# Kernel optimization log

Hardware: AMD Instinct MI355X
Metric: run time of the kernel (lower is better)

The kernel has to match this reference:

```python
import jax, jax.numpy as jnp
import numpy as np

EPS = 1e-5

def bn_eval(x, p):
    # p: [4, C] = gamma, beta, running_mean, running_var; channel-last broadcast
    g, b, m, v = p[0], p[1], p[2], p[3]
    return (x - m) * (g / jnp.sqrt(v + EPS)) + b

def _bn_params(k, c):
    k1, k2, k3, k4 = jax.random.split(k, 4)
    gamma = jax.random.uniform(k1, (c,)) + 0.5
    beta = jax.random.normal(k2, (c,)) * 0.1
    mean = jax.random.normal(k3, (c,)) * 0.1
    var = jax.random.uniform(k4, (c,)) + 0.5
    return jnp.stack([gamma, beta, mean, var])

def _lin(k, fan_in, fan_out):
    bound = 1.0 / np.sqrt(fan_in)
    kw, kb = jax.random.split(k)
    w = jax.random.uniform(kw, (fan_in, fan_out), minval=-bound, maxval=bound)
    b = jax.random.uniform(kb, (fan_out,), minval=-bound, maxval=bound)
    return w, b

def setup_inputs() -> dict:
    key = jax.random.key(0)
    B, N, S, C, G = 2, 4096, 16, 256, 8
    ks = jax.random.split(key, 20)
    feats = jax.random.normal(ks[0], (B, N, C), dtype=jnp.float32)
    coords = jax.random.normal(ks[1], (B, N, 3), dtype=jnp.float32)
    index = jax.random.randint(ks[2], (B, N, S), 0, N, dtype=jnp.int32)
    wq, bq = _lin(ks[3], C, C); bnq = _bn_params(ks[4], C)
    wk, bk = _lin(ks[5], C, C); bnk = _bn_params(ks[6], C)
    wv, bv = _lin(ks[7], C, C)
    pm_w1, pm_b1 = _lin(ks[8], 3, C); pm_bn = _bn_params(ks[9], C)
    pm_w2, pm_b2 = _lin(ks[10], C, C)
    pb_w1, pb_b1 = _lin(ks[11], 3, C); pb_bn = _bn_params(ks[12], C)
    pb_w2, pb_b2 = _lin(ks[13], C, C)
    we_w1, we_b1 = _lin(ks[14], C, G); we_bn = _bn_params(ks[15], G)
    we_w2, we_b2 = _lin(ks[16], G, G)
    return dict(feats=feats, coords=coords, index=index,
                wq=wq, bq=bq, bnq=bnq, wk=wk, bk=bk, bnk=bnk, wv=wv, bv=bv,
                pm_w1=pm_w1, pm_b1=pm_b1, pm_bn=pm_bn, pm_w2=pm_w2, pm_b2=pm_b2,
                pb_w1=pb_w1, pb_b1=pb_b1, pb_bn=pb_bn, pb_w2=pb_w2, pb_b2=pb_b2,
                we_w1=we_w1, we_b1=we_b1, we_bn=we_bn, we_w2=we_w2, we_b2=we_b2)

def reference(feats, coords, index,
              wq, bq, bnq, wk, bk, bnk, wv, bv,
              pm_w1, pm_b1, pm_bn, pm_w2, pm_b2,
              pb_w1, pb_b1, pb_bn, pb_w2, pb_b2,
              we_w1, we_b1, we_bn, we_w2, we_b2):
    B, N, C = feats.shape
    S = index.shape[2]
    G = we_w1.shape[1]
    q = jax.nn.relu(bn_eval(feats @ wq + bq, bnq))                       # [B,N,C]
    k = jax.nn.relu(bn_eval(feats @ wk + bk, bnk))                       # [B,N,C]
    v = feats @ wv + bv                                                   # [B,N,C]
    idx = index.reshape(B, N * S)
    key_g = jnp.take_along_axis(k, idx[:, :, None], axis=1).reshape(B, N, S, C)
    val_g = jnp.take_along_axis(v, idx[:, :, None], axis=1).reshape(B, N, S, C)
    crd_g = jnp.take_along_axis(coords, idx[:, :, None], axis=1).reshape(B, N, S, 3)
    relation_qk = key_g - q[:, :, None, :]                                # [B,N,S,C]
    pos = coords[:, :, None, :] - crd_g                                   # [B,N,S,3]
    pem = jax.nn.relu(bn_eval(pos @ pm_w1 + pm_b1, pm_bn)) @ pm_w2 + pm_b2
    relation_qk = relation_qk * pem
    peb = jax.nn.relu(bn_eval(pos @ pb_w1 + pb_b1, pb_bn)) @ pb_w2 + pb_b2
    relation_qk = relation_qk + peb
    val_g = val_g + peb
    w = jax.nn.relu(bn_eval(relation_qk @ we_w1 + we_b1, we_bn)) @ we_w2 + we_b2  # [B,N,S,G]
    w = jax.nn.softmax(w, axis=2)                                         # softmax over neighbors
    val_g = val_g.reshape(B, N, S, G, C // G)
    out = jnp.einsum('bnsgi,bnsg->bngi', val_g, w).reshape(B, N, C)
    return out
```

## Files before the change

kernel.cpp:

```cpp
#include <hip/hip_runtime.h>
#include <hip/hip_bf16.h>


typedef __attribute__((ext_vector_type(8))) short bf16x8_t;
typedef __attribute__((ext_vector_type(4))) float f32x4_t;

#define BN_EPS 1e-5f
#define WSYNC() asm volatile("s_waitcnt lgkmcnt(0)" ::: "memory")

__device__ __forceinline__ float blo(unsigned int v) {
    union { unsigned int u; float f; } x; x.u = v << 16; return x.f;
}
__device__ __forceinline__ float bhi(unsigned int v) {
    union { unsigned int u; float f; } x; x.u = v & 0xffff0000u; return x.f;
}
__device__ __forceinline__ unsigned int fbits(float f) {
    union { float f; unsigned int u; } x; x.f = f; return x.u;
}
__device__ __forceinline__ unsigned short f2b(float f) {
    unsigned int u = fbits(f);
    return (unsigned short)((u + 0x7fffu + ((u >> 16) & 1u)) >> 16);
}
__device__ __forceinline__ float b2f(unsigned short h) {
    union { unsigned int u; float f; } x; x.u = ((unsigned int)h) << 16; return x.f;
}
__device__ __forceinline__ unsigned int f2bpk(float a, float b) {
    union { __hip_bfloat162 h; unsigned int u; } x;
    x.h = __float22bfloat162_rn(make_float2(a, b));
    return x.u;
}
__device__ __forceinline__ unsigned int relpair(unsigned int kb, unsigned int qb,
                                                unsigned int pm_, unsigned int pb_) {
    float r0 = (blo(kb) - blo(qb)) * blo(pm_) + blo(pb_);
    float r1 = (bhi(kb) - bhi(qb)) * bhi(pm_) + bhi(pb_);
    return f2bpk(r0, r1);
}

__global__ __launch_bounds__(256) void k_prep(
    const float* __restrict__ wq, const float* __restrict__ wk,
    const float* __restrict__ wv, const float* __restrict__ pm2,
    const float* __restrict__ pb2,
    const float* __restrict__ pm_w1, const float* __restrict__ pm_b1,
    const float* __restrict__ pm_bn,
    const float* __restrict__ pb_w1, const float* __restrict__ pb_b1,
    const float* __restrict__ pb_bn,
    const float* __restrict__ we_w1,
    const float* __restrict__ bq, const float* __restrict__ bnq,
    const float* __restrict__ bk, const float* __restrict__ bnk,
    const float* __restrict__ bv,
    unsigned short* __restrict__ wsT, unsigned short* __restrict__ w1F,
    unsigned short* __restrict__ we1TF, float* __restrict__ SS)
{
    const int bid = blockIdx.x, t = threadIdx.x;
    if (bid < 160) {
        __shared__ unsigned short T[32][72];
        const int mat = bid >> 5;
        const int kk  = (bid >> 2) & 7;
        const int ntq = bid & 3;
        const float* s = (mat == 0) ? wq : (mat == 1) ? wk : (mat == 2) ? wv
                         : (mat == 3) ? pm2 : pb2;
        {
            int c = t & 63, r0 = t >> 6;
            for (int i = 0; i < 8; ++i) {
                int r = r0 + i * 4;
                T[r][c] = f2b(s[(kk * 32 + r) * 256 + ntq * 64 + c]);
            }
        }
        __syncthreads();
        {
            int seg = t >> 6, lane = t & 63;
            int col = seg * 16 + (lane & 15);
            int kr  = (lane >> 4) * 8;
            unsigned int v[8];
            #pragma unroll
            for (int j = 0; j < 8; ++j) v[j] = T[kr + j][col];
            uint4 o;
            o.x = v[0] | (v[1] << 16);
            o.y = v[2] | (v[3] << 16);
            o.z = v[4] | (v[5] << 16);
            o.w = v[6] | (v[7] << 16);
            *(uint4*)(wsT + mat * 65536 + (ntq * 4 + seg) * 4096 + kk * 512 + lane * 8) = o;
        }
    } else if (bid == 160) {
        int c = t;
        int nt = c >> 4, l15 = c & 15;
        float sm = pm_bn[c] / sqrtf(pm_bn[768 + c] + BN_EPS);
        float sb = pb_bn[c] / sqrtf(pb_bn[768 + c] + BN_EPS);
        float W[2][4];
        W[0][0] = pm_w1[c] * sm; W[0][1] = pm_w1[256 + c] * sm;
        W[0][2] = pm_w1[512 + c] * sm;
        W[0][3] = (pm_b1[c] - pm_bn[512 + c]) * sm + pm_bn[256 + c];
        W[1][0] = pb_w1[c] * sb; W[1][1] = pb_w1[256 + c] * sb;
        W[1][2] = pb_w1[512 + c] * sb;
        W[1][3] = (pb_b1[c] - pb_bn[512 + c]) * sb + pb_bn[256 + c];
        for (int pass = 0; pass < 2; ++pass) {
            unsigned short xh = f2b(W[pass][0]), xl = f2b(W[pass][0] - b2f(xh));
            unsigned short yh = f2b(W[pass][1]), yl = f2b(W[pass][1] - b2f(yh));
            unsigned short zh = f2b(W[pass][2]), zl = f2b(W[pass][2] - b2f(zh));
            unsigned short bh = f2b(W[pass][3]), bl = f2b(W[pass][3] - b2f(bh));
            unsigned short sl[16] = { xh, xh, xl, yh, yh, yl, zh, zh, zl,
                                      bh, bl, 0, 0, 0, 0, 0 };
            for (int q = 0; q < 4; ++q)
                for (int j = 0; j < 8; ++j)
                    w1F[((pass * 16 + nt) * 64 + q * 16 + l15) * 8 + j] =
                        (q < 2) ? sl[q * 8 + j] : (unsigned short)0;
        }
    } else {
        for (int j = 0; j < 8; ++j) {
            int e = t * 8 + j;
            int g = e >> 8, c = e & 255;
            we1TF[g * 256 + c] = f2b(we_w1[c * 8 + g]);
        }
        int c = t;
        float sq = bnq[c] / sqrtf(bnq[768 + c] + BN_EPS);
        SS[c]        = sq;
        SS[256 + c]  = (bq[c] - bnq[512 + c]) * sq + bnq[256 + c];
        float sk = bnk[c] / sqrtf(bnk[768 + c] + BN_EPS);
        SS[512 + c]  = sk;
        SS[768 + c]  = (bk[c] - bnk[512 + c]) * sk + bnk[256 + c];
        SS[1024 + c] = 1.0f;
        SS[1280 + c] = bv[c];
    }
}

__global__ __launch_bounds__(256) void k_qkv(
    const float* __restrict__ feats,
    const unsigned short* __restrict__ wT,
    const float* __restrict__ SS,
    unsigned short* __restrict__ qkv)
{
    __shared__ unsigned short A[32][264];
    const int t    = threadIdx.x;
    const int widx = blockIdx.x >> 8;
    const int mb   = blockIdx.x & 255;

    for (int i = 0; i < 8; ++i) {
        int row = 4 * i + (t >> 6), col = (t & 63) * 4;
        float4 f = *(const float4*)(feats + (mb * 32 + row) * 256 + col);
        *(uint2*)&A[row][col] = make_uint2(f2bpk(f.x, f.y), f2bpk(f.z, f.w));
    }
    __syncthreads();

    const int lane = t & 63, w = t >> 6;
    const int ln15 = lane & 15, quad = lane >> 4;
    const int mt = w & 1, nh = w >> 1;

    bf16x8_t afr[8];
    #pragma unroll
    for (int kk = 0; kk < 8; ++kk)
        afr[kk] = *(const bf16x8_t*)&A[mt * 16 + ln15][kk * 32 + quad * 8];

    const unsigned short* W = wT + widx * 65536;
    unsigned short* dst = qkv + (size_t)widx * 8192 * 256;

    f32x4_t acc[8];
    for (int j = 0; j < 8; ++j) acc[j] = (f32x4_t){0.f, 0.f, 0.f, 0.f};

    #pragma unroll
    for (int kk = 0; kk < 8; ++kk) {
        #pragma unroll
        for (int j = 0; j < 8; ++j) {
            int nt = nh * 8 + j;
            bf16x8_t wfr = *(const bf16x8_t*)(W + ((nt * 8 + kk) * 64 + lane) * 8);
            acc[j] = __builtin_amdgcn_mfma_f32_16x16x32_bf16(wfr, afr[kk], acc[j], 0, 0, 0);
        }
    }

    const float* S = SS + widx * 512;
    const int row = mb * 32 + mt * 16 + ln15;
    #pragma unroll
    for (int j = 0; j < 8; ++j) {
        int n0 = (nh * 8 + j) * 16 + quad * 4;
        float4 s4 = *(const float4*)(S + n0);
        float4 h4 = *(const float4*)(S + 256 + n0);
        float y0 = acc[j][0] * s4.x + h4.x;
        float y1 = acc[j][1] * s4.y + h4.y;
        float y2 = acc[j][2] * s4.z + h4.z;
        float y3 = acc[j][3] * s4.w + h4.w;
        if (widx < 2) {
            y0 = fmaxf(y0, 0.f); y1 = fmaxf(y1, 0.f);
            y2 = fmaxf(y2, 0.f); y3 = fmaxf(y3, 0.f);
        }
        *(uint2*)(dst + (size_t)row * 256 + n0) =
            make_uint2(f2bpk(y0, y1), f2bpk(y2, y3));
    }
}

__global__ __launch_bounds__(512, 4) void k_main(
    const float* __restrict__ coords,
    const int*   __restrict__ index,
    const unsigned short* __restrict__ qm,
    const unsigned short* __restrict__ km,
    const unsigned short* __restrict__ vm,
    const unsigned short* __restrict__ pmw2F,
    const unsigned short* __restrict__ pbw2F,
    const unsigned short* __restrict__ w1F,
    const unsigned short* __restrict__ we1TF,
    const float* __restrict__ pm_b2, const float* __restrict__ pb_b2,
    const float* __restrict__ we_b1, const float* __restrict__ we_bn,
    const float* __restrict__ we_w2, const float* __restrict__ we_b2,
    float* __restrict__ out)
{
    __shared__ unsigned short bufR[64][264];
    __shared__ unsigned short bufP[64][264];
    __shared__ unsigned short posX[64][32];
    __shared__ float usP[2][64][8];
    __shared__ float us_[64][10];
    __shared__ int   rowg_[64];
    __shared__ float we2s[8][8];
    __shared__ float web2[8], swe8[8], dwe8[8];

    const int t   = threadIdx.x;
    const int P0  = blockIdx.x * 4;
    const int bb_ = P0 >> 12;
    const int w = t >> 6, lane = t & 63;
    const int ln15 = lane & 15, quad = lane >> 4;
    const int p   = w >> 1, sub = w & 1;
    const int R0  = p * 16;
    const int Pg  = P0 + p;

    const int rg = (bb_ << 12) + index[Pg * 16 + ln15];

    if (t < 64) {
        int m  = t;
        int Pr = P0 + (m >> 4);
        int rs = (bb_ << 12) + index[Pr * 16 + (m & 15)];
        rowg_[m] = rs;
        float x = coords[Pr * 3 + 0] - coords[rs * 3 + 0];
        float y = coords[Pr * 3 + 1] - coords[rs * 3 + 1];
        float z = coords[Pr * 3 + 2] - coords[rs * 3 + 2];
        unsigned short xh = f2b(x), xl = f2b(x - b2f(xh));
        unsigned short yh = f2b(y), yl = f2b(y - b2f(yh));
        unsigned short zh = f2b(z), zl = f2b(z - b2f(zh));
        const unsigned short one = 0x3f80;
        posX[m][0] = xh; posX[m][1] = xl; posX[m][2] = xh;
        posX[m][3] = yh; posX[m][4] = yl; posX[m][5] = yh;
        posX[m][6] = zh; posX[m][7] = zl; posX[m][8] = zh;
        posX[m][9] = one; posX[m][10] = one;
        #pragma unroll
        for (int j2 = 11; j2 < 32; ++j2) posX[m][j2] = 0;
        we2s[m >> 3][m & 7] = we_w2[m];
    }
    if (t < 8) {
        float s = we_bn[t] / sqrtf(we_bn[24 + t] + BN_EPS);
        swe8[t] = s;
        dwe8[t] = (we_b1[t] - we_bn[16 + t]) * s + we_bn[8 + t];
        web2[t] = we_b2[t];
    }
    __syncthreads();

    bf16x8_t afrP[4];
    #pragma unroll
    for (int mt = 0; mt < 4; ++mt)
        afrP[mt] = *(const bf16x8_t*)&posX[mt * 16 + ln15][quad * 8];

    {
        f32x4_t hb[2][4];
        for (int ntl = 0; ntl < 2; ++ntl)
            for (int mt = 0; mt < 4; ++mt) hb[ntl][mt] = (f32x4_t){0.f, 0.f, 0.f, 0.f};
        #pragma unroll
        for (int ntl = 0; ntl < 2; ++ntl) {
            int nt = w * 2 + ntl;
            bf16x8_t wfr = *(const bf16x8_t*)(w1F + ((16 + nt) * 64 + lane) * 8);
            #pragma unroll
            for (int mt = 0; mt < 4; ++mt)
                hb[ntl][mt] = __builtin_amdgcn_mfma_f32_16x16x32_bf16(wfr, afrP[mt], hb[ntl][mt], 0, 0, 0);
        }
        #pragma unroll
        for (int ntl = 0; ntl < 2; ++ntl) {
            int cb = w * 32 + ntl * 16 + quad * 4;
            #pragma unroll
            for (int mt = 0; mt < 4; ++mt) {
                unsigned int pk0 = f2bpk(fmaxf(hb[ntl][mt][0], 0.f), fmaxf(hb[ntl][mt][1], 0.f));
                unsigned int pk1 = f2bpk(fmaxf(hb[ntl][mt][2], 0.f), fmaxf(hb[ntl][mt][3], 0.f));
                *(uint2*)&bufR[mt * 16 + ln15][cb] = make_uint2(pk0, pk1);
            }
        }
    }
    __syncthreads();

    f32x4_t accM[2][4];
    for (int ntl = 0; ntl < 2; ++ntl)
        for (int mt = 0; mt < 4; ++mt) accM[ntl][mt] = (f32x4_t){0.f, 0.f, 0.f, 0.f};
    #pragma unroll
    for (int ntl = 0; ntl < 2; ++ntl) {
        int nt = w * 2 + ntl;
        bf16x8_t wfr = *(const bf16x8_t*)(w1F + (nt * 64 + lane) * 8);
        #pragma unroll
        for (int mt = 0; mt < 4; ++mt)
            accM[ntl][mt] = __builtin_amdgcn_mfma_f32_16x16x32_bf16(wfr, afrP[mt], accM[ntl][mt], 0, 0, 0);
    }
    f32x4_t acc[2][4];
    {
        f32x4_t b0 = *(const f32x4_t*)(pb_b2 + (w * 2    ) * 16 + quad * 4);
        f32x4_t b1 = *(const f32x4_t*)(pb_b2 + (w * 2 + 1) * 16 + quad * 4);
        for (int mt = 0; mt < 4; ++mt) { acc[0][mt] = b0; acc[1][mt] = b1; }
    }
    __builtin_amdgcn_s_setprio(1);
    #pragma unroll
    for (int kk = 0; kk < 8; ++kk) {
        bf16x8_t afr[4];
        #pragma unroll
        for (int mt = 0; mt < 4; ++mt)
            afr[mt] = *(const bf16x8_t*)&bufR[mt * 16 + ln15][kk * 32 + quad * 8];
        #pragma unroll
        for (int ntl = 0; ntl < 2; ++ntl) {
            int nt = w * 2 + ntl;
            bf16x8_t wfr = *(const bf16x8_t*)(pbw2F + ((nt * 8 + kk) * 64 + lane) * 8);
            #pragma unroll
            for (int mt = 0; mt < 4; ++mt)
                acc[ntl][mt] = __builtin_amdgcn_mfma_f32_16x16x32_bf16(wfr, afr[mt], acc[ntl][mt], 0, 0, 0);
        }
    }
    __builtin_amdgcn_s_setprio(0);
    #pragma unroll
    for (int ntl = 0; ntl < 2; ++ntl) {
        int cb = w * 32 + ntl * 16 + quad * 4;
        #pragma unroll
        for (int mt = 0; mt < 4; ++mt) {
            unsigned int pk0 = f2bpk(acc[ntl][mt][0], acc[ntl][mt][1]);
            unsigned int pk1 = f2bpk(acc[ntl][mt][2], acc[ntl][mt][3]);
            *(uint2*)&bufP[mt * 16 + ln15][cb] = make_uint2(pk0, pk1);
        }
    }
    __syncthreads();

    #pragma unroll
    for (int ntl = 0; ntl < 2; ++ntl) {
        int cb = w * 32 + ntl * 16 + quad * 4;
        #pragma unroll
        for (int mt = 0; mt < 4; ++mt) {
            unsigned int pk0 = f2bpk(fmaxf(accM[ntl][mt][0], 0.f), fmaxf(accM[ntl][mt][1], 0.f));
            unsigned int pk1 = f2bpk(fmaxf(accM[ntl][mt][2], 0.f), fmaxf(accM[ntl][mt][3], 0.f));
            *(uint2*)&bufR[mt * 16 + ln15][cb] = make_uint2(pk0, pk1);
        }
    }
    __syncthreads();

    uint4 kpre[4];
    #pragma unroll
    for (int kk = 0; kk < 4; ++kk)
        kpre[kk] = *(const uint4*)(km + (size_t)rg * 256 + (sub * 4 + kk) * 32 + quad * 8);
    {
        f32x4_t b0 = *(const f32x4_t*)(pm_b2 + (w * 2    ) * 16 + quad * 4);
        f32x4_t b1 = *(const f32x4_t*)(pm_b2 + (w * 2 + 1) * 16 + quad * 4);
        for (int mt = 0; mt < 4; ++mt) { acc[0][mt] = b0; acc[1][mt] = b1; }
    }
    __builtin_amdgcn_s_setprio(1);
    #pragma unroll
    for (int kk = 0; kk < 8; ++kk) {
        bf16x8_t afr[4];
        #pragma unroll
        for (int mt = 0; mt < 4; ++mt)
            afr[mt] = *(const bf16x8_t*)&bufR[mt * 16 + ln15][kk * 32 + quad * 8];
        #pragma unroll
        for (int ntl = 0; ntl < 2; ++ntl) {
            int nt = w * 2 + ntl;
            bf16x8_t wfr = *(const bf16x8_t*)(pmw2F + ((nt * 8 + kk) * 64 + lane) * 8);
            #pragma unroll
            for (int mt = 0; mt < 4; ++mt)
                acc[ntl][mt] = __builtin_amdgcn_mfma_f32_16x16x32_bf16(wfr, afr[mt], acc[ntl][mt], 0, 0, 0);
        }
    }
    __builtin_amdgcn_s_setprio(0);
    __syncthreads();

    uint4 qpre[4];
    #pragma unroll
    for (int kk = 0; kk < 4; ++kk)
        qpre[kk] = *(const uint4*)(qm + (size_t)Pg * 256 + (sub * 4 + kk) * 32 + quad * 8);

    #pragma unroll
    for (int ntl = 0; ntl < 2; ++ntl) {
        int cb = w * 32 + ntl * 16 + quad * 4;
        #pragma unroll
        for (int mt = 0; mt < 4; ++mt) {
            unsigned int pk0 = f2bpk(acc[ntl][mt][0], acc[ntl][mt][1]);
            unsigned int pk1 = f2bpk(acc[ntl][mt][2], acc[ntl][mt][3]);
            *(uint2*)&bufR[mt * 16 + ln15][cb] = make_uint2(pk0, pk1);
        }
    }
    __syncthreads();

    {
        const bf16x8_t bz = {0, 0, 0, 0, 0, 0, 0, 0};
        f32x4_t lacc = {0.f, 0.f, 0.f, 0.f};
        #pragma unroll
        for (int kk = 0; kk < 4; ++kk) {
            int cb8 = (sub * 4 + kk) * 32 + quad * 8;
            uint4 pm4 = *(const uint4*)&bufR[R0 + ln15][cb8];
            uint4 pb4 = *(const uint4*)&bufP[R0 + ln15][cb8];
            uint4 q4  = qpre[kk];
            union { uint4 u; bf16x8_t v; } rr;
            rr.u.x = relpair(kpre[kk].x, q4.x, pm4.x, pb4.x);
            rr.u.y = relpair(kpre[kk].y, q4.y, pm4.y, pb4.y);
            rr.u.z = relpair(kpre[kk].z, q4.z, pm4.z, pb4.z);
            rr.u.w = relpair(kpre[kk].w, q4.w, pm4.w, pb4.w);
            bf16x8_t wfr = bz;
            if (ln15 < 8) wfr = *(const bf16x8_t*)(we1TF + ln15 * 256 + cb8);
            lacc = __builtin_amdgcn_mfma_f32_16x16x32_bf16(wfr, rr.v, lacc, 0, 0, 0);
        }
        if (quad < 2)
            *(f32x4_t*)&usP[sub][R0 + ln15][quad * 4] = lacc;
    }

    const int c5 = (sub * 64 + lane) * 2;
    unsigned int vpre[16];
    #pragma unroll
    for (int s = 0; s < 16; ++s) {
        int rv = rowg_[R0 + s];
        vpre[s] = *(const unsigned int*)(vm + (size_t)rv * 256 + c5);
    }
    __syncthreads();

    if (sub == 0) {
        int s  = lane & 15, gg = lane >> 4;
        int g0 = gg * 2;
        float2 ua = *(const float2*)&usP[0][R0 + s][g0];
        float2 ub = *(const float2*)&usP[1][R0 + s][g0];
        float2 sw = *(const float2*)&swe8[g0];
        float2 dw = *(const float2*)&dwe8[g0];
        float u0 = fmaxf((ua.x + ub.x) * sw.x + dw.x, 0.f);
        float u1 = fmaxf((ua.y + ub.y) * sw.y + dw.y, 0.f);
        float p0 = __shfl_xor(u0, 16), p1 = __shfl_xor(u1, 16);
        float q0 = __shfl_xor(u0, 32), q1 = __shfl_xor(u1, 32);
        float r0 = __shfl_xor(p0, 32), r1 = __shfl_xor(p1, 32);
        int ga = g0 ^ 2, gb = g0 ^ 4, gc = g0 ^ 6;
        float l0 = web2[g0], l1 = web2[g0 + 1];
        float2 wv2;
        wv2 = *(const float2*)&we2s[g0][g0];     l0 += u0 * wv2.x; l1 += u0 * wv2.y;
        wv2 = *(const float2*)&we2s[g0 + 1][g0]; l0 += u1 * wv2.x; l1 += u1 * wv2.y;
        wv2 = *(const float2*)&we2s[ga][g0];     l0 += p0 * wv2.x; l1 += p0 * wv2.y;
        wv2 = *(const float2*)&we2s[ga + 1][g0]; l0 += p1 * wv2.x; l1 += p1 * wv2.y;
        wv2 = *(const float2*)&we2s[gb][g0];     l0 += q0 * wv2.x; l1 += q0 * wv2.y;
        wv2 = *(const float2*)&we2s[gb + 1][g0]; l0 += q1 * wv2.x; l1 += q1 * wv2.y;
        wv2 = *(const float2*)&we2s[gc][g0];     l0 += r0 * wv2.x; l1 += r0 * wv2.y;
        wv2 = *(const float2*)&we2s[gc + 1][g0]; l0 += r1 * wv2.x; l1 += r1 * wv2.y;
        *(float2*)&us_[R0 + s][g0] = make_float2(l0, l1);
    }
    WSYNC();

    if (sub == 0) {
        int g = lane & 7, sh = lane >> 3;
        int s0 = sh * 2;
        float a = us_[R0 + s0][g], b = us_[R0 + s0 + 1][g];
        float mx = fmaxf(a, b);
        mx = fmaxf(mx, __shfl_xor(mx, 8));
        mx = fmaxf(mx, __shfl_xor(mx, 16));
        mx = fmaxf(mx, __shfl_xor(mx, 32));
        float ea = __expf(a - mx), eb = __expf(b - mx);
        float sm = ea + eb;
        sm += __shfl_xor(sm, 8);
        sm += __shfl_xor(sm, 16);
        sm += __shfl_xor(sm, 32);
        float inv = 1.f / sm;
        us_[R0 + s0][g]     = ea * inv;
        us_[R0 + s0 + 1][g] = eb * inv;
    }
    __syncthreads();

    {
        int g = c5 >> 5;
        float a0 = 0.f, a1 = 0.f;
        #pragma unroll
        for (int s = 0; s < 16; ++s) {
            float wv_ = us_[R0 + s][g];
            unsigned int v2 = vpre[s];
            unsigned int p2 = *(const unsigned int*)&bufP[R0 + s][c5];
            a0 += wv_ * (blo(v2) + blo(p2));
            a1 += wv_ * (bhi(v2) + bhi(p2));
        }
        *(float2*)(out + (size_t)Pg * 256 + c5) = make_float2(a0, a1);
    }
}

extern "C" void kernel_launch(void* const* d_in, const int* in_sizes, int n_in,
                              void* d_out, int out_size, void* d_ws, size_t ws_size,
                              hipStream_t stream)
{
    const float* feats  = (const float*)d_in[0];
    const float* coords = (const float*)d_in[1];
    const int*   index  = (const int*)d_in[2];
    const float* wq     = (const float*)d_in[3];
    const float* bq     = (const float*)d_in[4];
    const float* bnq    = (const float*)d_in[5];
    const float* wk     = (const float*)d_in[6];
    const float* bk     = (const float*)d_in[7];
    const float* bnk    = (const float*)d_in[8];
    const float* wv     = (const float*)d_in[9];
    const float* bv     = (const float*)d_in[10];
    const float* pm_w1  = (const float*)d_in[11];
    const float* pm_b1  = (const float*)d_in[12];
    const float* pm_bn  = (const float*)d_in[13];
    const float* pm_w2  = (const float*)d_in[14];
    const float* pm_b2  = (const float*)d_in[15];
    const float* pb_w1  = (const float*)d_in[16];
    const float* pb_b1  = (const float*)d_in[17];
    const float* pb_bn  = (const float*)d_in[18];
    const float* pb_w2  = (const float*)d_in[19];
    const float* pb_b2  = (const float*)d_in[20];
    const float* we_w1  = (const float*)d_in[21];
    const float* we_b1  = (const float*)d_in[22];
    const float* we_bn  = (const float*)d_in[23];
    const float* we_w2  = (const float*)d_in[24];
    const float* we_b2  = (const float*)d_in[25];

    unsigned short* qkv   = (unsigned short*)d_ws;
    unsigned short* wsT   = qkv + (size_t)3 * 8192 * 256;
    unsigned short* we1TF = wsT + 5 * 65536;
    unsigned short* w1F   = we1TF + 2048;
    float*          SS    = (float*)(w1F + 16384);

    const size_t need = (size_t)13281280;
    if (ws_size < need) {
        hipMemsetAsync(d_out, 0, (size_t)out_size * 4, stream);
        return;
    }

    k_prep<<<162,  256, 0, stream>>>(wq, wk, wv, pm_w2, pb_w2,
                                     pm_w1, pm_b1, pm_bn,
                                     pb_w1, pb_b1, pb_bn,
                                     we_w1,
                                     bq, bnq, bk, bnk, bv,
                                     wsT, w1F, we1TF, SS);
    k_qkv <<<768,  256, 0, stream>>>(feats, wsT, SS, qkv);
    k_main<<<2048, 512, 0, stream>>>(coords, index,
                                     qkv,
                                     qkv + (size_t)8192 * 256,
                                     qkv + (size_t)2 * 8192 * 256,
                                     wsT + 3 * 65536,
                                     wsT + 4 * 65536,
                                     w1F, we1TF,
                                     pm_b2, pb_b2,
                                     we_b1, we_bn, we_w2, we_b2,
                                     (float*)d_out);
}
```

Measured before the change: 185.7 us.

## Merge pem and peb positional MLP stages to cut block barriers

```diff
diff --git a/kernel.cpp b/kernel.cpp
--- a/kernel.cpp
+++ b/kernel.cpp
@@ -255,46 +255,49 @@
         afrP[mt] = *(const bf16x8_t*)&posX[mt * 16 + ln15][quad * 8];
 
     {
-        f32x4_t hb[2][4];
+        f32x4_t hbB[2][4], hbM[2][4];
         for (int ntl = 0; ntl < 2; ++ntl)
-            for (int mt = 0; mt < 4; ++mt) hb[ntl][mt] = (f32x4_t){0.f, 0.f, 0.f, 0.f};
+            for (int mt = 0; mt < 4; ++mt) {
+                hbB[ntl][mt] = (f32x4_t){0.f, 0.f, 0.f, 0.f};
+                hbM[ntl][mt] = (f32x4_t){0.f, 0.f, 0.f, 0.f};
+            }
         #pragma unroll
         for (int ntl = 0; ntl < 2; ++ntl) {
             int nt = w * 2 + ntl;
-            bf16x8_t wfr = *(const bf16x8_t*)(w1F + ((16 + nt) * 64 + lane) * 8);
+            bf16x8_t wfrB = *(const bf16x8_t*)(w1F + ((16 + nt) * 64 + lane) * 8);
+            bf16x8_t wfrM = *(const bf16x8_t*)(w1F + (nt * 64 + lane) * 8);
             #pragma unroll
-            for (int mt = 0; mt < 4; ++mt)
-                hb[ntl][mt] = __builtin_amdgcn_mfma_f32_16x16x32_bf16(wfr, afrP[mt], hb[ntl][mt], 0, 0, 0);
+            for (int mt = 0; mt < 4; ++mt) {
+                hbB[ntl][mt] = __builtin_amdgcn_mfma_f32_16x16x32_bf16(wfrB, afrP[mt], hbB[ntl][mt], 0, 0, 0);
+                hbM[ntl][mt] = __builtin_amdgcn_mfma_f32_16x16x32_bf16(wfrM, afrP[mt], hbM[ntl][mt], 0, 0, 0);
+            }
         }
         #pragma unroll
         for (int ntl = 0; ntl < 2; ++ntl) {
             int cb = w * 32 + ntl * 16 + quad * 4;
             #pragma unroll
             for (int mt = 0; mt < 4; ++mt) {
-                unsigned int pk0 = f2bpk(fmaxf(hb[ntl][mt][0], 0.f), fmaxf(hb[ntl][mt][1], 0.f));
-                unsigned int pk1 = f2bpk(fmaxf(hb[ntl][mt][2], 0.f), fmaxf(hb[ntl][mt][3], 0.f));
-                *(uint2*)&bufR[mt * 16 + ln15][cb] = make_uint2(pk0, pk1);
+                unsigned int b0 = f2bpk(fmaxf(hbB[ntl][mt][0], 0.f), fmaxf(hbB[ntl][mt][1], 0.f));
+                unsigned int b1 = f2bpk(fmaxf(hbB[ntl][mt][2], 0.f), fmaxf(hbB[ntl][mt][3], 0.f));
+                *(uint2*)&bufR[mt * 16 + ln15][cb] = make_uint2(b0, b1);
+                unsigned int m0 = f2bpk(fmaxf(hbM[ntl][mt][0], 0.f), fmaxf(hbM[ntl][mt][1], 0.f));
+                unsigned int m1 = f2bpk(fmaxf(hbM[ntl][mt][2], 0.f), fmaxf(hbM[ntl][mt][3], 0.f));
+                *(uint2*)&bufP[mt * 16 + ln15][cb] = make_uint2(m0, m1);
             }
         }
     }
     __syncthreads();
 
-    f32x4_t accM[2][4];
-    for (int ntl = 0; ntl < 2; ++ntl)
-        for (int mt = 0; mt < 4; ++mt) accM[ntl][mt] = (f32x4_t){0.f, 0.f, 0.f, 0.f};
-    #pragma unroll
-    for (int ntl = 0; ntl < 2; ++ntl) {
-        int nt = w * 2 + ntl;
-        bf16x8_t wfr = *(const bf16x8_t*)(w1F + (nt * 64 + lane) * 8);
-        #pragma unroll
-        for (int mt = 0; mt < 4; ++mt)
-            accM[ntl][mt] = __builtin_amdgcn_mfma_f32_16x16x32_bf16(wfr, afrP[mt], accM[ntl][mt], 0, 0, 0);
-    }
-    f32x4_t acc[2][4];
+    f32x4_t accB[2][4], accM[2][4];
     {
         f32x4_t b0 = *(const f32x4_t*)(pb_b2 + (w * 2    ) * 16 + quad * 4);
         f32x4_t b1 = *(const f32x4_t*)(pb_b2 + (w * 2 + 1) * 16 + quad * 4);
-        for (int mt = 0; mt < 4; ++mt) { acc[0][mt] = b0; acc[1][mt] = b1; }
+        f32x4_t m0 = *(const f32x4_t*)(pm_b2 + (w * 2    ) * 16 + quad * 4);
+        f32x4_t m1 = *(const f32x4_t*)(pm_b2 + (w * 2 + 1) * 16 + quad * 4);
+        for (int mt = 0; mt < 4; ++mt) {
+            accB[0][mt] = b0; accB[1][mt] = b1;
+            accM[0][mt] = m0; accM[1][mt] = m1;
+        }
     }
     __builtin_amdgcn_s_setprio(1);
     #pragma unroll
@@ -309,74 +312,50 @@
             bf16x8_t wfr = *(const bf16x8_t*)(pbw2F + ((nt * 8 + kk) * 64 + lane) * 8);
             #pragma unroll
             for (int mt = 0; mt < 4; ++mt)
-                acc[ntl][mt] = __builtin_amdgcn_mfma_f32_16x16x32_bf16(wfr, afr[mt], acc[ntl][mt], 0, 0, 0);
-        }
-    }
-    __builtin_amdgcn_s_setprio(0);
-    #pragma unroll
-    for (int ntl = 0; ntl < 2; ++ntl) {
-        int cb = w * 32 + ntl * 16 + quad * 4;
-        #pragma unroll
-        for (int mt = 0; mt < 4; ++mt) {
-            unsigned int pk0 = f2bpk(acc[ntl][mt][0], acc[ntl][mt][1]);
-            unsigned int pk1 = f2bpk(acc[ntl][mt][2], acc[ntl][mt][3]);
-            *(uint2*)&bufP[mt * 16 + ln15][cb] = make_uint2(pk0, pk1);
-        }
-    }
-    __syncthreads();
-
-    #pragma unroll
-    for (int ntl = 0; ntl < 2; ++ntl) {
-        int cb = w * 32 + ntl * 16 + quad * 4;
-        #pragma unroll
-        for (int mt = 0; mt < 4; ++mt) {
-            unsigned int pk0 = f2bpk(fmaxf(accM[ntl][mt][0], 0.f), fmaxf(accM[ntl][mt][1], 0.f));
-            unsigned int pk1 = f2bpk(fmaxf(accM[ntl][mt][2], 0.f), fmaxf(accM[ntl][mt][3], 0.f));
-            *(uint2*)&bufR[mt * 16 + ln15][cb] = make_uint2(pk0, pk1);
-        }
-    }
-    __syncthreads();
-
-    uint4 kpre[4];
-    #pragma unroll
-    for (int kk = 0; kk < 4; ++kk)
-        kpre[kk] = *(const uint4*)(km + (size_t)rg * 256 + (sub * 4 + kk) * 32 + quad * 8);
-    {
-        f32x4_t b0 = *(const f32x4_t*)(pm_b2 + (w * 2    ) * 16 + quad * 4);
-        f32x4_t b1 = *(const f32x4_t*)(pm_b2 + (w * 2 + 1) * 16 + quad * 4);
-        for (int mt = 0; mt < 4; ++mt) { acc[0][mt] = b0; acc[1][mt] = b1; }
-    }
-    __builtin_amdgcn_s_setprio(1);
+                accB[ntl][mt] = __builtin_amdgcn_mfma_f32_16x16x32_bf16(wfr, afr[mt], accB[ntl][mt], 0, 0, 0);
+        }
+    }
     #pragma unroll
     for (int kk = 0; kk < 8; ++kk) {
         bf16x8_t afr[4];
         #pragma unroll
         for (int mt = 0; mt < 4; ++mt)
-            afr[mt] = *(const bf16x8_t*)&bufR[mt * 16 + ln15][kk * 32 + quad * 8];
+            afr[mt] = *(const bf16x8_t*)&bufP[mt * 16 + ln15][kk * 32 + quad * 8];
         #pragma unroll
         for (int ntl = 0; ntl < 2; ++ntl) {
             int nt = w * 2 + ntl;
             bf16x8_t wfr = *(const bf16x8_t*)(pmw2F + ((nt * 8 + kk) * 64 + lane) * 8);
             #pragma unroll
             for (int mt = 0; mt < 4; ++mt)
-                acc[ntl][mt] = __builtin_amdgcn_mfma_f32_16x16x32_bf16(wfr, afr[mt], acc[ntl][mt], 0, 0, 0);
+                accM[ntl][mt] = __builtin_amdgcn_mfma_f32_16x16x32_bf16(wfr, afr[mt], accM[ntl][mt], 0, 0, 0);
         }
     }
     __builtin_amdgcn_s_setprio(0);
     __syncthreads();
-
-    uint4 qpre[4];
-    #pragma unroll
-    for (int kk = 0; kk < 4; ++kk)
-        qpre[kk] = *(const uint4*)(qm + (size_t)Pg * 256 + (sub * 4 + kk) * 32 + quad * 8);
 
     #pragma unroll
     for (int ntl = 0; ntl < 2; ++ntl) {
         int cb = w * 32 + ntl * 16 + quad * 4;
         #pragma unroll
         for (int mt = 0; mt < 4; ++mt) {
-            unsigned int pk0 = f2bpk(acc[ntl][mt][0], acc[ntl][mt][1]);
-            unsigned int pk1 = f2bpk(acc[ntl][mt][2], acc[ntl][mt][3]);
+            unsigned int pk0 = f2bpk(accB[ntl][mt][0], accB[ntl][mt][1]);
+            unsigned int pk1 = f2bpk(accB[ntl][mt][2], accB[ntl][mt][3]);
+            *(uint2*)&bufP[mt * 16 + ln15][cb] = make_uint2(pk0, pk1);
+        }
+    }
+    uint4 kpre[4], qpre[4];
+    #pragma unroll
+    for (int kk = 0; kk < 4; ++kk) {
+        kpre[kk] = *(const uint4*)(km + (size_t)rg * 256 + (sub * 4 + kk) * 32 + quad * 8);
+        qpre[kk] = *(const uint4*)(qm + (size_t)Pg * 256 + (sub * 4 + kk) * 32 + quad * 8);
+    }
+    #pragma unroll
+    for (int ntl = 0; ntl < 2; ++ntl) {
+        int cb = w * 32 + ntl * 16 + quad * 4;
+        #pragma unroll
+        for (int mt = 0; mt < 4; ++mt) {
+            unsigned int pk0 = f2bpk(accM[ntl][mt][0], accM[ntl][mt][1]);
+            unsigned int pk1 = f2bpk(accM[ntl][mt][2], accM[ntl][mt][3]);
             *(uint2*)&bufR[mt * 16 + ln15][cb] = make_uint2(pk0, pk1);
         }
     }
```

New measurement: 190.8 us. 2.7% more time.
